# Kernel optimization log

Measured on AMD Instinct MI355X. Metric: run time of the kernel, lower is better.

Reference implementation:

```python
import jax, jax.numpy as jnp
import numpy as np

B, Q, C, V = 512, 100, 81, 117  # batch, queries, obj classes (80+no-object), verbs
THRES, ALPHA, BETA = 0.7, 1.0, 0.5


def setup_inputs() -> dict:
    key = jax.random.key(0)
    k1, k2, k3, k4, k5, k6 = jax.random.split(key, 6)
    out_obj_logits = jax.random.normal(k1, (B, Q, C), jnp.float32)
    out_verb_logits = jax.random.normal(k2, (B, Q, V), jnp.float32)
    out_sub_boxes = jax.random.uniform(k3, (B, Q, 4), jnp.float32)
    out_obj_boxes = jax.random.uniform(k4, (B, Q, 4), jnp.float32)
    # correct_mat: binary verb-object compatibility [V, C-1] + ones column for no-object slot -> [V, C]
    cm = (jax.random.uniform(k5, (V, C - 1)) < 0.3).astype(jnp.float32)
    correct_mat = jnp.concatenate([cm, jnp.ones((V, 1), jnp.float32)], axis=1)
    target_sizes = jax.random.randint(k6, (B, 2), 480, 1334).astype(jnp.int64)
    return {
        'out_obj_logits': out_obj_logits,
        'out_verb_logits': out_verb_logits,
        'out_sub_boxes': out_sub_boxes,
        'out_obj_boxes': out_obj_boxes,
        'correct_mat': correct_mat,
        'target_sizes': target_sizes,
    }


def _box_cxcywh_to_xyxy(b):
    cx, cy, w, h = b[..., 0], b[..., 1], b[..., 2], b[..., 3]
    return jnp.stack([cx - 0.5 * w, cy - 0.5 * h, cx + 0.5 * w, cy + 0.5 * h], axis=-1)


def _pairwise_iou(boxes):  # boxes [Q,4] xyxy (pixel coords, +1 convention as in source)
    x1, y1, x2, y2 = boxes[:, 0], boxes[:, 1], boxes[:, 2], boxes[:, 3]
    area = (x2 - x1 + 1.0) * (y2 - y1 + 1.0)
    xx1 = jnp.maximum(x1[:, None], x1[None, :])
    yy1 = jnp.maximum(y1[:, None], y1[None, :])
    xx2 = jnp.minimum(x2[:, None], x2[None, :])
    yy2 = jnp.minimum(y2[:, None], y2[None, :])
    w = jnp.maximum(0.0, xx2 - xx1 + 1.0)
    h = jnp.maximum(0.0, yy2 - yy1 + 1.0)
    inter = w * h
    union = area[:, None] + area[None, :] - inter
    return inter / union


def _nms_one_image(sub_b, obj_b, obj_lab, max_scores):
    # Greedy pairwise triplet NMS. Grouping key in the source degenerates to the
    # object label alone (subject cat is constant, verb-label string identical),
    # so suppression applies only between detections with the same object label.
    order = jnp.argsort(-max_scores)
    sb, ob, lab = sub_b[order], obj_b[order], obj_lab[order]
    ovr = jnp.power(_pairwise_iou(sb), ALPHA) * jnp.power(_pairwise_iou(ob), BETA)
    upper = jnp.triu(jnp.ones((Q, Q), bool), 1)
    sup_mat = upper & (lab[:, None] == lab[None, :]) & (ovr > THRES)

    def body(i, supp):
        return supp | (sup_mat[i] & jnp.logical_not(supp[i]))

    supp = jax.lax.fori_loop(0, Q, body, jnp.zeros((Q,), bool))
    keep = jnp.zeros((Q,), bool).at[order].set(jnp.logical_not(supp))
    return keep  # in original query order


def reference(out_obj_logits, out_verb_logits, out_sub_boxes, out_obj_boxes, correct_mat, target_sizes):
    obj_prob = jax.nn.softmax(out_obj_logits, axis=-1)
    obj_scores = obj_prob[..., :-1].max(axis=-1)            # [B,Q]
    obj_labels = obj_prob[..., :-1].argmax(axis=-1)         # [B,Q]
    verb_scores = jax.nn.sigmoid(out_verb_logits)           # [B,Q,V]

    ts = target_sizes.astype(jnp.float32)
    img_h, img_w = ts[:, 0], ts[:, 1]
    scale_fct = jnp.stack([img_w, img_h, img_w, img_h], axis=1)  # [B,4]
    sub_boxes = _box_cxcywh_to_xyxy(out_sub_boxes) * scale_fct[:, None, :]
    obj_boxes = _box_cxcywh_to_xyxy(out_obj_boxes) * scale_fct[:, None, :]

    # masks[b,q,v] = correct_mat[v, obj_labels[b,q]]
    masks = correct_mat.T[obj_labels]                        # [B,Q,V]
    hoi_scores = verb_scores * obj_scores[..., None] * masks

    max_scores = hoi_scores.max(axis=-1)                     # [B,Q]
    keep = jax.vmap(_nms_one_image)(sub_boxes, obj_boxes, obj_labels, max_scores)
    return hoi_scores, obj_labels, sub_boxes, obj_boxes, keep
```

## Files before the change

### kernel.cpp

```cpp
#include <hip/hip_runtime.h>
#include <math.h>

#define Bn 512
#define Qn 100
#define Cn 81
#define Vn 117
#define NQ (Bn * Qn)

#define OFF_HOI  0
#define OFF_LAB  (NQ * Vn)
#define OFF_SUB  (OFF_LAB + NQ)
#define OFF_OBJ  (OFF_SUB + NQ * 4)
#define OFF_KEEP (OFF_OBJ + NQ * 4)

__device__ __forceinline__ float frcp(float x) { return __builtin_amdgcn_rcpf(x); }

__global__ __launch_bounds__(128) void cm_transpose(const float* __restrict__ cm,
                                                    float* __restrict__ cmT) {
    int c = blockIdx.x;
    int v = threadIdx.x;
    if (v < Vn) cmT[c * Vn + v] = cm[v * Cn + c];
}

__global__ __launch_bounds__(256) void hoi_k1(
    const float* __restrict__ obj_logits,
    const float* __restrict__ verb_logits,
    const float* __restrict__ sub_boxes,
    const float* __restrict__ obj_boxes,
    const float* __restrict__ cmT,
    const int*   __restrict__ target_sizes,
    float* __restrict__ out)
{
    __shared__ float L[16 * Cn];
    __shared__ float W[16 * Vn];

    const int tid  = threadIdx.x;
    const int base = blockIdx.x * 16;
    const int t    = tid & 15;
    const int g    = tid >> 4;
    const int idx  = base + g;
    const int b    = idx / Qn;

    {
        const float4* lgs = (const float4*)(obj_logits + (size_t)base * Cn);
        float4* Lv = (float4*)L;
        for (int i = tid; i < (16 * Cn) / 4; i += 256) Lv[i] = lgs[i];
        const float4* vls = (const float4*)(verb_logits + (size_t)base * Vn);
        float4* Wv = (float4*)W;
        for (int i = tid; i < (16 * Vn) / 4; i += 256) Wv[i] = vls[i];
    }
    __syncthreads();

    const float* lg = L + g * Cn;
    float l0 = lg[t], l1 = lg[t + 16], l2 = lg[t + 32], l3 = lg[t + 48], l4 = lg[t + 64];
    float l5 = lg[80];

    float v = l0; int vid = t;
    if (l1 > v) { v = l1; vid = t + 16; }
    if (l2 > v) { v = l2; vid = t + 32; }
    if (l3 > v) { v = l3; vid = t + 48; }
    if (l4 > v) { v = l4; vid = t + 64; }
    #pragma unroll
    for (int o = 8; o; o >>= 1) {
        float ov = __shfl_xor(v, o, 64);
        int   oi = __shfl_xor(vid, o, 64);
        if (ov > v || (ov == v && oi < vid)) { v = ov; vid = oi; }
    }

    float e = __expf(l0) + __expf(l1) + __expf(l2) + __expf(l3) + __expf(l4);
    #pragma unroll
    for (int o = 8; o; o >>= 1) e += __shfl_xor(e, o, 64);
    e += __expf(l5);

    const int   label     = vid;
    const float obj_score = __expf(v) * frcp(e);

    float* vrow = W + g * Vn;
    const float* crow = cmT + (size_t)label * Vn;

    float mx = 0.f;
    #pragma unroll
    for (int c = 0; c < 8; c++) {
        int col = t + 16 * c;
        if (col < Vn) {
            float x = vrow[col];
            float h = frcp(1.f + __expf(-x)) * obj_score * crow[col];
            vrow[col] = h;
            mx = fmaxf(mx, h);
        }
    }
    #pragma unroll
    for (int o = 8; o; o >>= 1) mx = fmaxf(mx, __shfl_xor(mx, o, 64));

    if (t == 0) {
        out[OFF_LAB + idx]  = (float)label;
        out[OFF_KEEP + idx] = mx;
    }

    if (t < 2) {
        float ih = (float)target_sizes[2 * b + 0];
        float iw = (float)target_sizes[2 * b + 1];
        const float4 bx = ((const float4*)(t == 0 ? sub_boxes : obj_boxes))[idx];
        float4 r;
        r.x = (bx.x - 0.5f * bx.z) * iw;
        r.y = (bx.y - 0.5f * bx.w) * ih;
        r.z = (bx.x + 0.5f * bx.z) * iw;
        r.w = (bx.y + 0.5f * bx.w) * ih;
        ((float4*)(out + (t == 0 ? OFF_SUB : OFF_OBJ)))[idx] = r;
    }
    __syncthreads();

    {
        const float4* Wv = (const float4*)W;
        float4* ho = (float4*)(out + OFF_HOI + (size_t)base * Vn);
        for (int i = tid; i < (16 * Vn) / 4; i += 256) ho[i] = Wv[i];
    }
}

__global__ __launch_bounds__(128) void hoi_nms(float* __restrict__ out)
{
    __shared__ float  sc[Qn];
    __shared__ float4 SB[Qn], OB[Qn];
    __shared__ float  AS[Qn], AO[Qn];
    __shared__ int    LB[128];
    __shared__ int    OI[Qn];
    __shared__ unsigned long long ROW[Qn][2];

    const int b = blockIdx.x;
    const int t = threadIdx.x;
    const int w = t >> 6;

    float* keepp = out + OFF_KEEP + (size_t)b * Qn;

    if (t < Qn) { sc[t] = keepp[t]; ROW[t][0] = 0ull; ROW[t][1] = 0ull; }
    if (t >= Qn) LB[t] = -1;
    __syncthreads();

    if (t < Qn) {
        float s = sc[t];
        int r = 0;
        for (int j = 0; j < Qn; j++) {
            float sj = sc[j];
            r += (sj > s) || (sj == s && j < t);
        }
        float4 sb = ((const float4*)(out + OFF_SUB))[b * Qn + t];
        float4 ob = ((const float4*)(out + OFF_OBJ))[b * Qn + t];
        SB[r] = sb; OB[r] = ob;
        AS[r] = (sb.z - sb.x + 1.f) * (sb.w - sb.y + 1.f);
        AO[r] = (ob.z - ob.x + 1.f) * (ob.w - ob.y + 1.f);
        LB[r] = (int)out[OFF_LAB + b * Qn + t];
        OI[r] = t;
    }
    __syncthreads();

    const int  j  = t;
    const bool jv = (j < Qn);
    float4 js, jo; float jas = 0.f, jao = 0.f; int jlb = -2;
    js = make_float4(0.f, 0.f, 0.f, 0.f); jo = js;
    if (jv) { js = SB[j]; jo = OB[j]; jas = AS[j]; jao = AO[j]; jlb = LB[j]; }

    const int iend = (w == 0) ? 63 : 99;
    for (int i = 0; i < iend; i++) {
        float4 is = SB[i], io = OB[i];
        float  ias = AS[i], iao = AO[i];
        int    ilb = LB[i];
        float ww = fmaxf(0.f, fminf(is.z, js.z) - fmaxf(is.x, js.x) + 1.f);
        float hh = fmaxf(0.f, fminf(is.w, js.w) - fmaxf(is.y, js.y) + 1.f);
        float inter = ww * hh;
        float iou_s = inter / (ias + jas - inter);
        ww = fmaxf(0.f, fminf(io.z, jo.z) - fmaxf(io.x, jo.x) + 1.f);
        hh = fmaxf(0.f, fminf(io.w, jo.w) - fmaxf(io.y, jo.y) + 1.f);
        inter = ww * hh;
        float iou_o = inter / (iao + jao - inter);
        bool cond = jv && (j > i) && (jlb == ilb) && (iou_s * sqrtf(iou_o) > 0.7f);
        unsigned long long m = __ballot(cond);
        if ((t & 63) == 0) ROW[i][w] = m;
    }
    __syncthreads();

    unsigned long long s0 = 0ull, s1 = 0ull;
    #pragma unroll
    for (int i = 0; i < Qn - 1; i++) {
        unsigned long long dead = ((i < 64 ? s0 : s1) >> (i & 63)) & 1ull;
        unsigned long long msk  = dead - 1ull;
        s0 |= ROW[i][0] & msk;
        s1 |= ROW[i][1] & msk;
    }

    if (t < Qn) {
        unsigned long long bit = (t < 64 ? (s0 >> t) : (s1 >> (t - 64))) & 1ull;
        keepp[OI[t]] = bit ? 0.f : 1.f;
    }
}

extern "C" void kernel_launch(void* const* d_in, const int* in_sizes, int n_in,
                              void* d_out, int out_size, void* d_ws, size_t ws_size,
                              hipStream_t stream) {
    const float* obj_logits   = (const float*)d_in[0];
    const float* verb_logits  = (const float*)d_in[1];
    const float* sub_boxes    = (const float*)d_in[2];
    const float* obj_boxes    = (const float*)d_in[3];
    const float* correct_mat  = (const float*)d_in[4];
    const int*   target_sizes = (const int*)d_in[5];
    float* out = (float*)d_out;
    float* cmT = (float*)d_ws;

    cm_transpose<<<Cn, 128, 0, stream>>>(correct_mat, cmT);
    hoi_k1<<<NQ / 16, 256, 0, stream>>>(obj_logits, verb_logits, sub_boxes,
                                        obj_boxes, cmT, target_sizes, out);
    hoi_nms<<<Bn, 128, 0, stream>>>(out);
}
```

Baseline: 137.5 us.

## Split NMS into sort, parallel suppression-matrix, and chain kernels

Replaces the single per-image NMS kernel with three kernels. One ranks detections by score and writes them to workspace, one computes the suppression bitmask matrix across 8 blocks per image, and one resolves the greedy chain with a single wavefront. The aim is to expose far more parallelism than 512 blocks of serial row computation, and to skip row ORs for suppressed rows. The cost is extra kernel launches and global-memory round trips through workspace.

```diff
diff --git a/kernel.cpp b/kernel.cpp
--- a/kernel.cpp
+++ b/kernel.cpp
@@ -12,6 +12,9 @@
 #define OFF_SUB  (OFF_LAB + NQ)
 #define OFF_OBJ  (OFF_SUB + NQ * 4)
 #define OFF_KEEP (OFF_OBJ + NQ * 4)
+
+#define WS_SRT_OFF  65536
+#define WS_ROW_OFF  (65536 + Bn * 300 * 16)
 
 __device__ __forceinline__ float frcp(float x) { return __builtin_amdgcn_rcpf(x); }
 
@@ -117,80 +120,101 @@
     }
 }
 
-__global__ __launch_bounds__(128) void hoi_nms(float* __restrict__ out)
-{
-    __shared__ float  sc[Qn];
-    __shared__ float4 SB[Qn], OB[Qn];
-    __shared__ float  AS[Qn], AO[Qn];
-    __shared__ int    LB[128];
-    __shared__ int    OI[Qn];
-    __shared__ unsigned long long ROW[Qn][2];
-
+__global__ __launch_bounds__(128) void nms_sort(const float* __restrict__ out,
+                                                float4* __restrict__ srt)
+{
+    __shared__ float sc[Qn];
     const int b = blockIdx.x;
     const int t = threadIdx.x;
-    const int w = t >> 6;
-
-    float* keepp = out + OFF_KEEP + (size_t)b * Qn;
-
-    if (t < Qn) { sc[t] = keepp[t]; ROW[t][0] = 0ull; ROW[t][1] = 0ull; }
-    if (t >= Qn) LB[t] = -1;
-    __syncthreads();
-
+
+    float  kv = 0.f, labf = 0.f;
+    float4 sb = make_float4(0.f,0.f,0.f,0.f), ob = sb;
     if (t < Qn) {
-        float s = sc[t];
+        kv   = out[OFF_KEEP + b * Qn + t];
+        sb   = ((const float4*)(out + OFF_SUB))[b * Qn + t];
+        ob   = ((const float4*)(out + OFF_OBJ))[b * Qn + t];
+        labf = out[OFF_LAB + b * Qn + t];
+        sc[t] = kv;
+    }
+    __syncthreads();
+
+    if (t < Qn) {
         int r = 0;
+        #pragma unroll 4
         for (int j = 0; j < Qn; j++) {
             float sj = sc[j];
-            r += (sj > s) || (sj == s && j < t);
+            r += (sj > kv) || (sj == kv && j < t);
         }
-        float4 sb = ((const float4*)(out + OFF_SUB))[b * Qn + t];
-        float4 ob = ((const float4*)(out + OFF_OBJ))[b * Qn + t];
-        SB[r] = sb; OB[r] = ob;
-        AS[r] = (sb.z - sb.x + 1.f) * (sb.w - sb.y + 1.f);
-        AO[r] = (ob.z - ob.x + 1.f) * (ob.w - ob.y + 1.f);
-        LB[r] = (int)out[OFF_LAB + b * Qn + t];
-        OI[r] = t;
-    }
-    __syncthreads();
-
-    const int  j  = t;
-    const bool jv = (j < Qn);
-    float4 js, jo; float jas = 0.f, jao = 0.f; int jlb = -2;
-    js = make_float4(0.f, 0.f, 0.f, 0.f); jo = js;
-    if (jv) { js = SB[j]; jo = OB[j]; jas = AS[j]; jao = AO[j]; jlb = LB[j]; }
-
-    const int iend = (w == 0) ? 63 : 99;
-    for (int i = 0; i < iend; i++) {
-        float4 is = SB[i], io = OB[i];
-        float  ias = AS[i], iao = AO[i];
-        int    ilb = LB[i];
+        float4* S = srt + (size_t)b * 300;
+        S[r]           = sb;
+        S[100 + r]     = ob;
+        S[200 + r]     = make_float4(
+            (sb.z - sb.x + 1.f) * (sb.w - sb.y + 1.f),
+            (ob.z - ob.x + 1.f) * (ob.w - ob.y + 1.f),
+            labf, (float)t);
+    }
+}
+
+__global__ __launch_bounds__(128) void nms_mat(const float4* __restrict__ srt,
+                                               unsigned long long* __restrict__ roww)
+{
+    const int g = blockIdx.x >> 9;
+    const int b = blockIdx.x & 511;
+    const int t = threadIdx.x;
+    const int sub  = t >> 6;
+    const int lane = t & 63;
+    const bool jv  = (t < Qn);
+
+    const float4* S = srt + (size_t)b * 300;
+    float4 js = make_float4(0.f,0.f,0.f,0.f), jo = js, jm = js;
+    if (jv) { js = S[t]; jo = S[100 + t]; jm = S[200 + t]; }
+
+    const int i0 = g * 13;
+    const int i1 = (i0 + 13 < Qn - 1) ? i0 + 13 : Qn - 1;
+    unsigned long long* rw = roww + ((size_t)b * Qn) * 2;
+
+    for (int i = i0; i < i1; i++) {
+        float4 is = S[i], io = S[100 + i], im = S[200 + i];
         float ww = fmaxf(0.f, fminf(is.z, js.z) - fmaxf(is.x, js.x) + 1.f);
         float hh = fmaxf(0.f, fminf(is.w, js.w) - fmaxf(is.y, js.y) + 1.f);
         float inter = ww * hh;
-        float iou_s = inter / (ias + jas - inter);
+        float iou_s = inter / (im.x + jm.x - inter);
         ww = fmaxf(0.f, fminf(io.z, jo.z) - fmaxf(io.x, jo.x) + 1.f);
         hh = fmaxf(0.f, fminf(io.w, jo.w) - fmaxf(io.y, jo.y) + 1.f);
         inter = ww * hh;
-        float iou_o = inter / (iao + jao - inter);
-        bool cond = jv && (j > i) && (jlb == ilb) && (iou_s * sqrtf(iou_o) > 0.7f);
+        float iou_o = inter / (im.y + jm.y - inter);
+        bool cond = jv && (t > i) && (jm.z == im.z) && (iou_s * sqrtf(iou_o) > 0.7f);
         unsigned long long m = __ballot(cond);
-        if ((t & 63) == 0) ROW[i][w] = m;
-    }
+        if (lane == 0) rw[2 * i + sub] = m;
+    }
+}
+
+__global__ __launch_bounds__(64) void nms_chain(const float4* __restrict__ srt,
+                                                const ulonglong2* __restrict__ roww2,
+                                                float* __restrict__ out)
+{
+    __shared__ ulonglong2 R[Qn];
+    __shared__ int oi[Qn];
+    const int b = blockIdx.x;
+    const int l = threadIdx.x;
+
+    const ulonglong2* rw = roww2 + (size_t)b * Qn;
+    const float4*     M  = srt + (size_t)b * 300 + 200;
+
+    R[l] = rw[l];
+    oi[l] = (int)M[l].w;
+    if (l < 36) { R[64 + l] = rw[64 + l]; oi[64 + l] = (int)M[64 + l].w; }
     __syncthreads();
 
     unsigned long long s0 = 0ull, s1 = 0ull;
-    #pragma unroll
-    for (int i = 0; i < Qn - 1; i++) {
-        unsigned long long dead = ((i < 64 ? s0 : s1) >> (i & 63)) & 1ull;
-        unsigned long long msk  = dead - 1ull;
-        s0 |= ROW[i][0] & msk;
-        s1 |= ROW[i][1] & msk;
-    }
-
-    if (t < Qn) {
-        unsigned long long bit = (t < 64 ? (s0 >> t) : (s1 >> (t - 64))) & 1ull;
-        keepp[OI[t]] = bit ? 0.f : 1.f;
-    }
+    for (int k = 0; k < Qn - 1; k++) {
+        unsigned long long dead = ((k < 64 ? s0 : s1) >> (k & 63)) & 1ull;
+        if (!dead) { ulonglong2 r = R[k]; s0 |= r.x; s1 |= r.y; }
+    }
+
+    float* keepp = out + OFF_KEEP + (size_t)b * Qn;
+    keepp[oi[l]] = ((s0 >> l) & 1ull) ? 0.f : 1.f;
+    if (l < 36) keepp[oi[64 + l]] = ((s1 >> l) & 1ull) ? 0.f : 1.f;
 }
 
 extern "C" void kernel_launch(void* const* d_in, const int* in_sizes, int n_in,
@@ -203,10 +227,15 @@
     const float* correct_mat  = (const float*)d_in[4];
     const int*   target_sizes = (const int*)d_in[5];
     float* out = (float*)d_out;
-    float* cmT = (float*)d_ws;
+
+    float*              cmT  = (float*)d_ws;
+    float4*             srt  = (float4*)((char*)d_ws + WS_SRT_OFF);
+    unsigned long long* roww = (unsigned long long*)((char*)d_ws + WS_ROW_OFF);
 
     cm_transpose<<<Cn, 128, 0, stream>>>(correct_mat, cmT);
     hoi_k1<<<NQ / 16, 256, 0, stream>>>(obj_logits, verb_logits, sub_boxes,
                                         obj_boxes, cmT, target_sizes, out);
-    hoi_nms<<<Bn, 128, 0, stream>>>(out);
-}
+    nms_sort<<<Bn, 128, 0, stream>>>(out, srt);
+    nms_mat<<<8 * Bn, 128, 0, stream>>>(srt, roww);
+    nms_chain<<<Bn, 64, 0, stream>>>(srt, (const ulonglong2*)roww, out);
+}
```

After: 130.1 us (median of 2 runs). 5.4% less time.
